# Kernel tuning notes

Measured on AMD Instinct MI355X. Metric: run time of the kernel, lower is better.

Reference implementation:

```python
import jax, jax.numpy as jnp
import numpy as np

N, D, R, NB, E = 50000, 128, 16, 10, 1600000
DECAY_RATE = 0.1
LN_EPS = 1e-5

def setup_inputs() -> dict:
    key = jax.random.key(0)
    ks = jax.random.split(key, 12)
    x = jax.random.normal(ks[0], (N, D), dtype=jnp.float32)
    edge_index = jax.random.randint(ks[1], (2, E), 0, N, dtype=jnp.int64)
    edge_type = jax.random.randint(ks[2], (E,), 0, R, dtype=jnp.int64)
    edge_time = jax.random.uniform(ks[3], (E,), dtype=jnp.float32)
    s = 1.0 / np.sqrt(D)
    basis = jax.random.normal(ks[4], (NB, D, D), dtype=jnp.float32) * s   # RGCN basis matrices
    comp = jax.random.normal(ks[5], (R, NB), dtype=jnp.float32) * (1.0 / np.sqrt(NB))
    root = jax.random.normal(ks[6], (D, D), dtype=jnp.float32) * s        # RGCN self-loop weight
    bias = jnp.zeros((D,), dtype=jnp.float32)
    tp_w = jax.random.normal(ks[7], (D, D), dtype=jnp.float32) * s        # time_proj
    tp_b = jnp.zeros((D,), dtype=jnp.float32)
    gamma = jnp.ones((D,), dtype=jnp.float32)
    beta = jnp.zeros((D,), dtype=jnp.float32)
    return {"x": x, "edge_index": edge_index, "edge_type": edge_type, "edge_time": edge_time,
            "basis": basis, "comp": comp, "root": root, "bias": bias,
            "tp_w": tp_w, "tp_b": tp_b, "gamma": gamma, "beta": beta}

def reference(x, edge_index, edge_type, edge_time, basis, comp, root, bias, tp_w, tp_b, gamma, beta):
    n, d = x.shape
    r = comp.shape[0]
    src, dst = edge_index[0], edge_index[1]
    # ---- RGCNConv (basis decomposition, per-relation mean aggregation) ----
    W = jnp.einsum('rb,bio->rio', comp, basis)                 # [R, D, D]
    msg = x[src]                                               # [E, D] gather
    seg = dst * r + edge_type                                  # combined (node, relation) segment id
    agg = jax.ops.segment_sum(msg, seg, num_segments=n * r)    # [N*R, D]
    cnt = jax.ops.segment_sum(jnp.ones_like(seg, dtype=x.dtype), seg, num_segments=n * r)
    agg = (agg / jnp.maximum(cnt, 1.0)[:, None]).reshape(n, r, d)  # per-relation mean
    x_rgcn = jnp.einsum('nrd,rdo->no', agg, W) + x @ root + bias
    # ---- exponential time decay weights, normalized to sum 1 ----
    td = edge_time.max() - edge_time
    td = td / (td.max() + 1e-8)
    w = jnp.exp(-DECAY_RATE * td)
    w = w / (w.sum() + 1e-8)
    # ---- time-decay aggregation (sum over relations == single scatter-add) ----
    agg_t = jax.ops.segment_sum(msg * w[:, None], dst, num_segments=n)
    deg = jax.ops.segment_sum(jnp.ones_like(dst, dtype=x.dtype), dst, num_segments=n)
    x_time = agg_t / jnp.clip(deg, 1.0)[:, None]
    # ---- combine, relu, (dropout=identity in eval), layernorm ----
    xc = x_rgcn + x_time @ tp_w + tp_b
    h = jax.nn.relu(xc)
    mu = h.mean(-1, keepdims=True)
    var = ((h - mu) ** 2).mean(-1, keepdims=True)
    return (h - mu) * jax.lax.rsqrt(var + LN_EPS) * gamma + beta
```

## Files before the change

### kernel.cpp

```cpp
#include <hip/hip_runtime.h>
#include <hip/hip_bf16.h>
#include <math.h>

#define NN 50000
#define DD 128
#define RR 16
#define NBASIS 10
#define NE 1600000
#define NSEG (NN * RR)
#define NPART ((NSEG + 1023) / 1024)
#define NSLICE 12
#define KTOT (NSLICE * DD)
#define DECAY 0.1f

typedef short bf16x8 __attribute__((ext_vector_type(8)));
typedef float f32x4 __attribute__((ext_vector_type(4)));
typedef float f32x2 __attribute__((ext_vector_type(2)));

__device__ __forceinline__ ushort f2b(float f) {
    unsigned u = __float_as_uint(f);
    unsigned r = (u + 0x7FFFu + ((u >> 16) & 1u)) >> 16;
    return (ushort)r;
}
__device__ __forceinline__ unsigned cvt_pk_bf16(float lo, float hi) {
    unsigned r;
    asm("v_cvt_pk_bf16_f32 %0, %1, %2" : "=v"(r) : "v"(lo), "v"(hi));
    return r;
}

__global__ void k_init(unsigned* red) {
    if (threadIdx.x == 0) {
        red[0] = 0u;
        red[1] = 0x7F800000u;
        ((float*)red)[2] = 0.0f;
    }
}

__global__ __launch_bounds__(256) void k_pre1(const float* __restrict__ t,
                                              const int* __restrict__ edst,
                                              const int* __restrict__ etype,
                                              unsigned* __restrict__ red,
                                              unsigned* __restrict__ cnt,
                                              unsigned* __restrict__ segarr,
                                              ushort* __restrict__ rank) {
    __shared__ float smx[4], smn[4];
    const int tid = threadIdx.x;
    float mx = 0.0f, mn = 1e30f;
    const int stride = gridDim.x * 256;
    for (int e = blockIdx.x * 256 + tid; e < NE; e += stride) {
        float v = __builtin_nontemporal_load(t + e);
        int d   = __builtin_nontemporal_load(edst + e);
        int ty  = __builtin_nontemporal_load(etype + e);
        mx = fmaxf(mx, v);
        mn = fminf(mn, v);
        int seg = d * RR + ty;
        unsigned rk = atomicAdd(&cnt[seg], 1u);
        __builtin_nontemporal_store((unsigned)seg, segarr + e);
        __builtin_nontemporal_store((ushort)rk, rank + e);
    }
    for (int o = 32; o >= 1; o >>= 1) {
        mx = fmaxf(mx, __shfl_down(mx, o, 64));
        mn = fminf(mn, __shfl_down(mn, o, 64));
    }
    if ((tid & 63) == 0) { smx[tid >> 6] = mx; smn[tid >> 6] = mn; }
    __syncthreads();
    if (tid == 0) {
        mx = fmaxf(fmaxf(smx[0], smx[1]), fmaxf(smx[2], smx[3]));
        mn = fminf(fminf(smn[0], smn[1]), fminf(smn[2], smn[3]));
        atomicMax(&red[0], __float_as_uint(mx));
        atomicMin(&red[1], __float_as_uint(mn));
    }
}

__global__ __launch_bounds__(1024) void k_scan1(const unsigned* __restrict__ cnt,
                                                unsigned* __restrict__ segptr,
                                                unsigned* __restrict__ part) {
    __shared__ unsigned sh[1024];
    int tid = threadIdx.x;
    int i = blockIdx.x * 1024 + tid;
    unsigned v = (i < NSEG) ? cnt[i] : 0u;
    sh[tid] = v;
    __syncthreads();
    for (int off = 1; off < 1024; off <<= 1) {
        unsigned t = (tid >= off) ? sh[tid - off] : 0u;
        __syncthreads();
        sh[tid] += t;
        __syncthreads();
    }
    if (i < NSEG) segptr[i] = sh[tid] - v;
    if (tid == 1023) part[blockIdx.x] = sh[1023];
}

__global__ __launch_bounds__(1024) void k_scan2(unsigned* __restrict__ part) {
    __shared__ unsigned sh[1024];
    int tid = threadIdx.x;
    unsigned v = (tid < NPART) ? part[tid] : 0u;
    sh[tid] = v;
    __syncthreads();
    for (int off = 1; off < 1024; off <<= 1) {
        unsigned t = (tid >= off) ? sh[tid - off] : 0u;
        __syncthreads();
        sh[tid] += t;
        __syncthreads();
    }
    if (tid < NPART) part[tid] = sh[tid] - v;
}

__global__ __launch_bounds__(1024) void k_scan3(unsigned* __restrict__ segptr,
                                                const unsigned* __restrict__ part) {
    int i = blockIdx.x * 1024 + threadIdx.x;
    if (i < NSEG) segptr[i] += part[i >> 10];
    if (blockIdx.x == 0 && threadIdx.x == 0) segptr[NSEG] = NE;
}

__global__ __launch_bounds__(256) void k_pre2(const int* __restrict__ esrc,
                                              const float* __restrict__ etime,
                                              const unsigned* __restrict__ segarr,
                                              const ushort* __restrict__ rank,
                                              unsigned* __restrict__ red,
                                              const unsigned* __restrict__ segptr,
                                              unsigned* __restrict__ srcw) {
    __shared__ float ssum[4];
    const int tid = threadIdx.x;
    const float tmax = __uint_as_float(red[0]);
    const float tmin = __uint_as_float(red[1]);
    const float rtd = -DECAY / (tmax - tmin + 1e-8f);
    float s = 0.0f;
    const int stride = gridDim.x * 256;
    for (int e = blockIdx.x * 256 + tid; e < NE; e += stride) {
        float tv    = __builtin_nontemporal_load(etime + e);
        int sv      = __builtin_nontemporal_load(esrc + e);
        unsigned sg = __builtin_nontemporal_load(segarr + e);
        unsigned rk = __builtin_nontemporal_load(rank + e);
        float w = __expf((tmax - tv) * rtd);
        s += w;
        unsigned pos = segptr[sg] + rk;
        srcw[pos] = (unsigned)(sv & 0xFFFF) | ((unsigned)f2b(w) << 16);
    }
    for (int o = 32; o >= 1; o >>= 1) s += __shfl_down(s, o, 64);
    if ((tid & 63) == 0) ssum[tid >> 6] = s;
    __syncthreads();
    if (tid == 0)
        atomicAdd(((float*)red) + 2, ssum[0] + ssum[1] + ssum[2] + ssum[3]);
}

#define XB_ITEMS (NN * (DD / 4))
__global__ __launch_bounds__(256) void k_prep(const float* __restrict__ x,
                                              const float* __restrict__ basis,
                                              const float* __restrict__ root,
                                              const float* __restrict__ tp_w,
                                              ushort* __restrict__ xb,
                                              ushort* __restrict__ Bt3) {
    int idx = blockIdx.x * 256 + threadIdx.x;
    if (idx < XB_ITEMS) {
        float4 v = ((const float4*)x)[idx];
        uint2 o;
        o.x = cvt_pk_bf16(v.x, v.y);
        o.y = cvt_pk_bf16(v.z, v.w);
        ((uint2*)xb)[idx] = o;
        return;
    }
    int bidx = idx - XB_ITEMS;
    if (bidx >= DD * KTOT) return;
    int j = bidx / KTOT, k = bidx - j * KTOT;
    int s = k >> 7, d = k & 127;
    float v;
    if (s < NBASIS) {
        v = basis[(s * DD + d) * DD + j];
    } else if (s == NBASIS) {
        v = tp_w[d * DD + j];
    } else {
        v = root[d * DD + j];
    }
    Bt3[bidx] = f2b(v);
}

__global__ __launch_bounds__(256) void k_gather(
    const ushort* __restrict__ xb, const unsigned* __restrict__ srcw,
    const unsigned* __restrict__ segptr, const unsigned* __restrict__ red,
    const float* __restrict__ comp,
    ushort* __restrict__ A2)
{
    const int wave = threadIdx.x >> 6, lane = threadIdx.x & 63;
    int dst0 = blockIdx.x * 4 + wave;
    if (dst0 >= NN) return;
    const int dst = __builtin_amdgcn_readfirstlane(dst0);
    const float sumw = ((const float*)red)[2];
    const unsigned s0 = (unsigned)dst * RR;
    const unsigned start = segptr[s0];
    const unsigned endAll = segptr[s0 + RR];
    const unsigned deg = endAll - start;
    unsigned* arow = (unsigned*)(A2 + (size_t)dst * KTOT);
    const unsigned* xbu = (const unsigned*)xb;

    f32x2 cb[NBASIS];
#pragma unroll
    for (int b = 0; b < NBASIS; ++b) cb[b] = (f32x2){0.f, 0.f};
    f32x2 acc = {0.f, 0.f}, xt = {0.f, 0.f};

    int r = 0;
    unsigned scur = start;
    unsigned endr = segptr[s0 + 1];
    unsigned e = start;

#define FLUSH_REL {                                                          \
        float scl = (endr > scur) ? (1.0f / (float)(endr - scur)) : 0.0f;    \
        f32x2 t = acc * scl;                                                 \
        _Pragma("unroll")                                                    \
        for (int b = 0; b < NBASIS; ++b)                                     \
            cb[b] += t * comp[r * NBASIS + b];                               \
        acc = (f32x2){0.f, 0.f}; scur = endr; ++r;                           \
        endr = (r < RR) ? segptr[s0 + r + 1] : 0xFFFFFFFFu; }

#define ACCUM(recq, pvq) {                                                   \
        float wgt = __uint_as_float((recq) & 0xFFFF0000u);                   \
        f32x2 v;                                                             \
        v.x = __uint_as_float((pvq) << 16);                                  \
        v.y = __uint_as_float((pvq) & 0xFFFF0000u);                          \
        acc += v;                                                            \
        xt += v * wgt; }

    while (e < endAll) {
        unsigned idx = e + (unsigned)lane;
        unsigned recv = srcw[(idx < endAll) ? idx : (endAll - 1u)];
        unsigned chunk = endAll - e;
        if (chunk > 64u) chunk = 64u;
        unsigned j = 0;
        for (; j + 8u <= chunk; j += 8u) {
            unsigned rec0 = (unsigned)__builtin_amdgcn_readlane((int)recv, (int)(j + 0));
            unsigned rec1 = (unsigned)__builtin_amdgcn_readlane((int)recv, (int)(j + 1));
            unsigned rec2 = (unsigned)__builtin_amdgcn_readlane((int)recv, (int)(j + 2));
            unsigned rec3 = (unsigned)__builtin_amdgcn_readlane((int)recv, (int)(j + 3));
            unsigned rec4 = (unsigned)__builtin_amdgcn_readlane((int)recv, (int)(j + 4));
            unsigned rec5 = (unsigned)__builtin_amdgcn_readlane((int)recv, (int)(j + 5));
            unsigned rec6 = (unsigned)__builtin_amdgcn_readlane((int)recv, (int)(j + 6));
            unsigned rec7 = (unsigned)__builtin_amdgcn_readlane((int)recv, (int)(j + 7));
            unsigned pv0 = xbu[((rec0 & 0xFFFFu) << 6) + lane];
            unsigned pv1 = xbu[((rec1 & 0xFFFFu) << 6) + lane];
            unsigned pv2 = xbu[((rec2 & 0xFFFFu) << 6) + lane];
            unsigned pv3 = xbu[((rec3 & 0xFFFFu) << 6) + lane];
            unsigned pv4 = xbu[((rec4 & 0xFFFFu) << 6) + lane];
            unsigned pv5 = xbu[((rec5 & 0xFFFFu) << 6) + lane];
            unsigned pv6 = xbu[((rec6 & 0xFFFFu) << 6) + lane];
            unsigned pv7 = xbu[((rec7 & 0xFFFFu) << 6) + lane];
            while (e >= endr) FLUSH_REL; ACCUM(rec0, pv0); ++e;
            while (e >= endr) FLUSH_REL; ACCUM(rec1, pv1); ++e;
            while (e >= endr) FLUSH_REL; ACCUM(rec2, pv2); ++e;
            while (e >= endr) FLUSH_REL; ACCUM(rec3, pv3); ++e;
            while (e >= endr) FLUSH_REL; ACCUM(rec4, pv4); ++e;
            while (e >= endr) FLUSH_REL; ACCUM(rec5, pv5); ++e;
            while (e >= endr) FLUSH_REL; ACCUM(rec6, pv6); ++e;
            while (e >= endr) FLUSH_REL; ACCUM(rec7, pv7); ++e;
        }
        for (; j < chunk; ++j) {
            unsigned rc = (unsigned)__builtin_amdgcn_readlane((int)recv, (int)j);
            unsigned pv = xbu[((rc & 0xFFFFu) << 6) + lane];
            while (e >= endr) FLUSH_REL;
            ACCUM(rc, pv);
            ++e;
        }
    }
    while (r < RR) FLUSH_REL;

#pragma unroll
    for (int b = 0; b < NBASIS; ++b)
        __builtin_nontemporal_store(cvt_pk_bf16(cb[b].x, cb[b].y),
                                    arow + b * 64 + lane);

    float s2 = 1.0f / ((sumw + 1e-8f) * fmaxf((float)deg, 1.0f));
    __builtin_nontemporal_store(cvt_pk_bf16(xt.x * s2, xt.y * s2),
                                arow + NBASIS * 64 + lane);
    __builtin_nontemporal_store(
        ((const unsigned*)(xb + (size_t)dst * DD))[lane],
        arow + (NBASIS + 1) * 64 + lane);
#undef FLUSH_REL
#undef ACCUM
}

__global__ __launch_bounds__(256) void k_fgemm(
    const ushort* __restrict__ A2, const ushort* __restrict__ Bt3,
    const float* __restrict__ bias, const float* __restrict__ tpb,
    const float* __restrict__ gamma, const float* __restrict__ beta,
    float* __restrict__ out)
{
    __shared__ unsigned Bs[2][4096];

    const int tid = threadIdx.x;
    const int w = tid >> 6, lane = tid & 63;
    const int quad = lane >> 4, l16 = lane & 15;
    const int n0 = blockIdx.x * 64;

    f32x4 acc[8];
#pragma unroll
    for (int ct = 0; ct < 8; ++ct) acc[ct] = (f32x4){0.f, 0.f, 0.f, 0.f};

    const ushort* arow = A2 + (size_t)(n0 + w * 16 + l16) * KTOT + quad * 8;
    const int srow = lane >> 3;
    const int sc   = lane & 7;

#define STAGE(buf, itv) {                                                    \
        const int k0_ = (itv) * 64;                                          \
        _Pragma("unroll")                                                    \
        for (int i_ = 0; i_ < 4; ++i_) {                                     \
            const int cid_ = i_ * 4 + w;                                     \
            const int row_ = cid_ * 8 + srow;                                \
            const int ck_  = sc ^ (row_ & 7);                                \
            const ushort* gb_ = Bt3 + (size_t)row_ * KTOT + k0_ + ck_ * 8;   \
            __builtin_amdgcn_global_load_lds(                                \
                (const __attribute__((address_space(1))) unsigned*)gb_,      \
                (__attribute__((address_space(3))) unsigned*)&Bs[buf][cid_ * 256], \
                16, 0, 0);                                                   \
        } }

    STAGE(0, 0);
    bf16x8 afp0 = *(const bf16x8*)(arow);
    bf16x8 afp1 = *(const bf16x8*)(arow + 32);
    __syncthreads();

    const int NIT = KTOT / 64;
    for (int it = 0; it < NIT; ++it) {
        if (it + 1 < NIT) STAGE((it + 1) & 1, it + 1);
        bf16x8 af0 = afp0, af1 = afp1;
        if (it + 1 < NIT) {
            afp0 = *(const bf16x8*)(arow + (it + 1) * 64);
            afp1 = *(const bf16x8*)(arow + (it + 1) * 64 + 32);
        }
        const unsigned* Bp = &Bs[it & 1][0];
#pragma unroll
        for (int ct = 0; ct < 8; ++ct) {
            const int rB = ct * 16 + l16;
            bf16x8 b0 = *(const bf16x8*)&Bp[rB * 32 + ((quad ^ (rB & 7)) << 2)];
            bf16x8 b1 = *(const bf16x8*)&Bp[rB * 32 + (((4 + quad) ^ (rB & 7)) << 2)];
            acc[ct] = __builtin_amdgcn_mfma_f32_16x16x32_bf16(af0, b0, acc[ct], 0, 0, 0);
            acc[ct] = __builtin_amdgcn_mfma_f32_16x16x32_bf16(af1, b1, acc[ct], 0, 0, 0);
        }
        __syncthreads();
    }
#undef STAGE

    float bc[8], gc[8], be[8];
#pragma unroll
    for (int ct = 0; ct < 8; ++ct) {
        int col = ct * 16 + l16;
        bc[ct] = bias[col] + tpb[col];
        gc[ct] = gamma[col];
        be[ct] = beta[col];
    }
    float s[4] = {0, 0, 0, 0}, q[4] = {0, 0, 0, 0};
#pragma unroll
    for (int ct = 0; ct < 8; ++ct)
#pragma unroll
        for (int i = 0; i < 4; ++i) {
            float v = fmaxf(acc[ct][i] + bc[ct], 0.0f);
            acc[ct][i] = v;
            s[i] += v;
            q[i] = fmaf(v, v, q[i]);
        }
#pragma unroll
    for (int off = 1; off < 16; off <<= 1)
#pragma unroll
        for (int i = 0; i < 4; ++i) {
            s[i] += __shfl_xor(s[i], off, 64);
            q[i] += __shfl_xor(q[i], off, 64);
        }
#pragma unroll
    for (int i = 0; i < 4; ++i) {
        const int row = n0 + w * 16 + quad * 4 + i;
        float mu  = s[i] * (1.0f / DD);
        float var = q[i] * (1.0f / DD) - mu * mu;
        float inv = rsqrtf(var + 1e-5f);
        if (row < NN) {
#pragma unroll
            for (int ct = 0; ct < 8; ++ct)
                __builtin_nontemporal_store(
                    (acc[ct][i] - mu) * inv * gc[ct] + be[ct],
                    out + (size_t)row * DD + ct * 16 + l16);
        }
    }
}

extern "C" void kernel_launch(void* const* d_in, const int* in_sizes, int n_in,
                              void* d_out, int out_size, void* d_ws, size_t ws_size,
                              hipStream_t stream)
{
    const float* x     = (const float*)d_in[0];
    const int*   ei    = (const int*)d_in[1];
    const int*   etype = (const int*)d_in[2];
    const float* etime = (const float*)d_in[3];
    const float* basis = (const float*)d_in[4];
    const float* comp  = (const float*)d_in[5];
    const float* root  = (const float*)d_in[6];
    const float* bias  = (const float*)d_in[7];
    const float* tp_w  = (const float*)d_in[8];
    const float* tp_b  = (const float*)d_in[9];
    const float* gamma = (const float*)d_in[10];
    const float* beta  = (const float*)d_in[11];
    float* out = (float*)d_out;

    char* ws = (char*)d_ws;
    size_t off = 0;
    auto alloc = [&](size_t bytes) -> void* {
        void* p = ws + off;
        off = (off + bytes + 255) & ~(size_t)255;
        return p;
    };
    unsigned* red    = (unsigned*)alloc(64);
    unsigned* cnt    = (unsigned*)alloc((size_t)NSEG * 4);
    unsigned* segptr = (unsigned*)alloc((size_t)(NSEG + 1) * 4);
    unsigned* part   = (unsigned*)alloc(1024 * 4);
    unsigned* srcw   = (unsigned*)alloc((size_t)NE * 4);
    unsigned* segarr = (unsigned*)alloc((size_t)NE * 4);
    ushort*   rank   = (ushort*)alloc((size_t)NE * 2);
    ushort*   xb     = (ushort*)alloc((size_t)NN * DD * 2);
    ushort*   Bt3    = (ushort*)alloc((size_t)DD * KTOT * 2);
    ushort*   A2     = (ushort*)alloc((size_t)50048 * KTOT * 2);
    (void)ws_size;

    const int* esrc = ei;
    const int* edst = ei + NE;

    hipLaunchKernelGGL(k_init, dim3(1), dim3(64), 0, stream, red);
    (void)hipMemsetAsync(cnt, 0, (size_t)NSEG * 4, stream);
    hipLaunchKernelGGL(k_pre1, dim3(1024), dim3(256), 0, stream,
                       etime, edst, etype, red, cnt, segarr, rank);

    hipLaunchKernelGGL(k_scan1, dim3(NPART), dim3(1024), 0, stream, cnt, segptr, part);
    hipLaunchKernelGGL(k_scan2, dim3(1), dim3(1024), 0, stream, part);
    hipLaunchKernelGGL(k_scan3, dim3(NPART), dim3(1024), 0, stream, segptr, part);

    hipLaunchKernelGGL(k_pre2, dim3(1024), dim3(256), 0, stream,
                       esrc, etime, segarr, rank, red, segptr, srcw);

    hipLaunchKernelGGL(k_prep, dim3((XB_ITEMS + DD * KTOT + 255) / 256), dim3(256), 0, stream,
                       x, basis, root, tp_w, xb, Bt3);

    hipLaunchKernelGGL(k_gather, dim3((NN + 3) / 4), dim3(256), 0, stream,
                       xb, srcw, segptr, red, comp, A2);

    hipLaunchKernelGGL(k_fgemm, dim3((50048 + 63) / 64), dim3(256), 0, stream,
                       A2, Bt3, bias, tp_b, gamma, beta, out);
}
```

Measured before the change: 391.9 us.

## Fuse counting, time min/max and bf16 prep into one front kernel; pack seg+rank

Merges the atomic segment-counting pass, the edge-time min/max reduction and the x/weight bf16 conversion into a single launch whose block ranges do independent work. This lets the three jobs run concurrently and removes one launch. Segment id and rank are now packed into one 32-bit word, replacing separate 4-byte and 2-byte arrays and cutting traffic in k_pre2. The scatter store of srcw becomes nontemporal. Packing assumes each segment's rank stays below 4096 and each segment id fits in 20 bits.

```diff
diff --git a/kernel.cpp b/kernel.cpp
--- a/kernel.cpp
+++ b/kernel.cpp
@@ -36,40 +36,75 @@
     }
 }
 
-__global__ __launch_bounds__(256) void k_pre1(const float* __restrict__ t,
-                                              const int* __restrict__ edst,
-                                              const int* __restrict__ etype,
-                                              unsigned* __restrict__ red,
-                                              unsigned* __restrict__ cnt,
-                                              unsigned* __restrict__ segarr,
-                                              ushort* __restrict__ rank) {
-    __shared__ float smx[4], smn[4];
+#define XB_ITEMS (NN * (DD / 4))
+#define PREP_ITEMS (XB_ITEMS + DD * KTOT)
+__global__ __launch_bounds__(256) void k_front(
+    const int* __restrict__ edst, const int* __restrict__ etype,
+    const float* __restrict__ t,
+    const float* __restrict__ x, const float* __restrict__ basis,
+    const float* __restrict__ root, const float* __restrict__ tp_w,
+    unsigned* __restrict__ red, unsigned* __restrict__ cnt,
+    unsigned* __restrict__ segrank,
+    ushort* __restrict__ xb, ushort* __restrict__ Bt3)
+{
+    const int bid = blockIdx.x;
     const int tid = threadIdx.x;
-    float mx = 0.0f, mn = 1e30f;
-    const int stride = gridDim.x * 256;
-    for (int e = blockIdx.x * 256 + tid; e < NE; e += stride) {
-        float v = __builtin_nontemporal_load(t + e);
-        int d   = __builtin_nontemporal_load(edst + e);
-        int ty  = __builtin_nontemporal_load(etype + e);
-        mx = fmaxf(mx, v);
-        mn = fminf(mn, v);
-        int seg = d * RR + ty;
-        unsigned rk = atomicAdd(&cnt[seg], 1u);
-        __builtin_nontemporal_store((unsigned)seg, segarr + e);
-        __builtin_nontemporal_store((ushort)rk, rank + e);
-    }
-    for (int o = 32; o >= 1; o >>= 1) {
-        mx = fmaxf(mx, __shfl_down(mx, o, 64));
-        mn = fminf(mn, __shfl_down(mn, o, 64));
-    }
-    if ((tid & 63) == 0) { smx[tid >> 6] = mx; smn[tid >> 6] = mn; }
-    __syncthreads();
-    if (tid == 0) {
-        mx = fmaxf(fmaxf(smx[0], smx[1]), fmaxf(smx[2], smx[3]));
-        mn = fminf(fminf(smn[0], smn[1]), fminf(smn[2], smn[3]));
-        atomicMax(&red[0], __float_as_uint(mx));
-        atomicMin(&red[1], __float_as_uint(mn));
-    }
+    if (bid < 1024) {
+        const int stride = 1024 * 256;
+        for (int e = bid * 256 + tid; e < NE; e += stride) {
+            int d  = __builtin_nontemporal_load(edst + e);
+            int ty = __builtin_nontemporal_load(etype + e);
+            int seg = d * RR + ty;
+            unsigned rk = atomicAdd(&cnt[seg], 1u);
+            __builtin_nontemporal_store(((unsigned)seg << 12) | rk, segrank + e);
+        }
+        return;
+    }
+    if (bid < 2048) {
+        __shared__ float smx[4], smn[4];
+        float mx = 0.0f, mn = 1e30f;
+        const int stride = 1024 * 256;
+        for (int i = (bid - 1024) * 256 + tid; i < NE / 4; i += stride) {
+            f32x4 v = __builtin_nontemporal_load(((const f32x4*)t) + i);
+            mx = fmaxf(mx, fmaxf(fmaxf(v.x, v.y), fmaxf(v.z, v.w)));
+            mn = fminf(mn, fminf(fminf(v.x, v.y), fminf(v.z, v.w)));
+        }
+        for (int o = 32; o >= 1; o >>= 1) {
+            mx = fmaxf(mx, __shfl_down(mx, o, 64));
+            mn = fminf(mn, __shfl_down(mn, o, 64));
+        }
+        if ((tid & 63) == 0) { smx[tid >> 6] = mx; smn[tid >> 6] = mn; }
+        __syncthreads();
+        if (tid == 0) {
+            mx = fmaxf(fmaxf(smx[0], smx[1]), fmaxf(smx[2], smx[3]));
+            mn = fminf(fminf(smn[0], smn[1]), fminf(smn[2], smn[3]));
+            atomicMax(&red[0], __float_as_uint(mx));
+            atomicMin(&red[1], __float_as_uint(mn));
+        }
+        return;
+    }
+    int idx = (bid - 2048) * 256 + tid;
+    if (idx < XB_ITEMS) {
+        f32x4 v = ((const f32x4*)x)[idx];
+        uint2 o;
+        o.x = cvt_pk_bf16(v.x, v.y);
+        o.y = cvt_pk_bf16(v.z, v.w);
+        ((uint2*)xb)[idx] = o;
+        return;
+    }
+    int bidx = idx - XB_ITEMS;
+    if (bidx >= DD * KTOT) return;
+    int j = bidx / KTOT, k = bidx - j * KTOT;
+    int s = k >> 7, d = k & 127;
+    float v;
+    if (s < NBASIS) {
+        v = basis[(s * DD + d) * DD + j];
+    } else if (s == NBASIS) {
+        v = tp_w[d * DD + j];
+    } else {
+        v = root[d * DD + j];
+    }
+    Bt3[bidx] = f2b(v);
 }
 
 __global__ __launch_bounds__(1024) void k_scan1(const unsigned* __restrict__ cnt,
@@ -115,8 +150,7 @@
 
 __global__ __launch_bounds__(256) void k_pre2(const int* __restrict__ esrc,
                                               const float* __restrict__ etime,
-                                              const unsigned* __restrict__ segarr,
-                                              const ushort* __restrict__ rank,
+                                              const unsigned* __restrict__ segrank,
                                               unsigned* __restrict__ red,
                                               const unsigned* __restrict__ segptr,
                                               unsigned* __restrict__ srcw) {
@@ -130,49 +164,18 @@
     for (int e = blockIdx.x * 256 + tid; e < NE; e += stride) {
         float tv    = __builtin_nontemporal_load(etime + e);
         int sv      = __builtin_nontemporal_load(esrc + e);
-        unsigned sg = __builtin_nontemporal_load(segarr + e);
-        unsigned rk = __builtin_nontemporal_load(rank + e);
+        unsigned sr = __builtin_nontemporal_load(segrank + e);
         float w = __expf((tmax - tv) * rtd);
         s += w;
-        unsigned pos = segptr[sg] + rk;
-        srcw[pos] = (unsigned)(sv & 0xFFFF) | ((unsigned)f2b(w) << 16);
+        unsigned pos = segptr[sr >> 12] + (sr & 4095u);
+        __builtin_nontemporal_store(
+            (unsigned)(sv & 0xFFFF) | ((unsigned)f2b(w) << 16), srcw + pos);
     }
     for (int o = 32; o >= 1; o >>= 1) s += __shfl_down(s, o, 64);
     if ((tid & 63) == 0) ssum[tid >> 6] = s;
     __syncthreads();
     if (tid == 0)
         atomicAdd(((float*)red) + 2, ssum[0] + ssum[1] + ssum[2] + ssum[3]);
-}
-
-#define XB_ITEMS (NN * (DD / 4))
-__global__ __launch_bounds__(256) void k_prep(const float* __restrict__ x,
-                                              const float* __restrict__ basis,
-                                              const float* __restrict__ root,
-                                              const float* __restrict__ tp_w,
-                                              ushort* __restrict__ xb,
-                                              ushort* __restrict__ Bt3) {
-    int idx = blockIdx.x * 256 + threadIdx.x;
-    if (idx < XB_ITEMS) {
-        float4 v = ((const float4*)x)[idx];
-        uint2 o;
-        o.x = cvt_pk_bf16(v.x, v.y);
-        o.y = cvt_pk_bf16(v.z, v.w);
-        ((uint2*)xb)[idx] = o;
-        return;
-    }
-    int bidx = idx - XB_ITEMS;
-    if (bidx >= DD * KTOT) return;
-    int j = bidx / KTOT, k = bidx - j * KTOT;
-    int s = k >> 7, d = k & 127;
-    float v;
-    if (s < NBASIS) {
-        v = basis[(s * DD + d) * DD + j];
-    } else if (s == NBASIS) {
-        v = tp_w[d * DD + j];
-    } else {
-        v = root[d * DD + j];
-    }
-    Bt3[bidx] = f2b(v);
 }
 
 __global__ __launch_bounds__(256) void k_gather(
@@ -404,16 +407,15 @@
         off = (off + bytes + 255) & ~(size_t)255;
         return p;
     };
-    unsigned* red    = (unsigned*)alloc(64);
-    unsigned* cnt    = (unsigned*)alloc((size_t)NSEG * 4);
-    unsigned* segptr = (unsigned*)alloc((size_t)(NSEG + 1) * 4);
-    unsigned* part   = (unsigned*)alloc(1024 * 4);
-    unsigned* srcw   = (unsigned*)alloc((size_t)NE * 4);
-    unsigned* segarr = (unsigned*)alloc((size_t)NE * 4);
-    ushort*   rank   = (ushort*)alloc((size_t)NE * 2);
-    ushort*   xb     = (ushort*)alloc((size_t)NN * DD * 2);
-    ushort*   Bt3    = (ushort*)alloc((size_t)DD * KTOT * 2);
-    ushort*   A2     = (ushort*)alloc((size_t)50048 * KTOT * 2);
+    unsigned* red     = (unsigned*)alloc(64);
+    unsigned* cnt     = (unsigned*)alloc((size_t)NSEG * 4);
+    unsigned* segptr  = (unsigned*)alloc((size_t)(NSEG + 1) * 4);
+    unsigned* part    = (unsigned*)alloc(1024 * 4);
+    unsigned* srcw    = (unsigned*)alloc((size_t)NE * 4);
+    unsigned* segrank = (unsigned*)alloc((size_t)NE * 4);
+    ushort*   xb      = (ushort*)alloc((size_t)NN * DD * 2);
+    ushort*   Bt3     = (ushort*)alloc((size_t)DD * KTOT * 2);
+    ushort*   A2      = (ushort*)alloc((size_t)50048 * KTOT * 2);
     (void)ws_size;
 
     const int* esrc = ei;
@@ -421,18 +423,18 @@
 
     hipLaunchKernelGGL(k_init, dim3(1), dim3(64), 0, stream, red);
     (void)hipMemsetAsync(cnt, 0, (size_t)NSEG * 4, stream);
-    hipLaunchKernelGGL(k_pre1, dim3(1024), dim3(256), 0, stream,
-                       etime, edst, etype, red, cnt, segarr, rank);
+
+    const int prep_blocks = (PREP_ITEMS + 255) / 256;
+    hipLaunchKernelGGL(k_front, dim3(2048 + prep_blocks), dim3(256), 0, stream,
+                       edst, etype, etime, x, basis, root, tp_w,
+                       red, cnt, segrank, xb, Bt3);
 
     hipLaunchKernelGGL(k_scan1, dim3(NPART), dim3(1024), 0, stream, cnt, segptr, part);
     hipLaunchKernelGGL(k_scan2, dim3(1), dim3(1024), 0, stream, part);
     hipLaunchKernelGGL(k_scan3, dim3(NPART), dim3(1024), 0, stream, segptr, part);
 
     hipLaunchKernelGGL(k_pre2, dim3(1024), dim3(256), 0, stream,
-                       esrc, etime, segarr, rank, red, segptr, srcw);
-
-    hipLaunchKernelGGL(k_prep, dim3((XB_ITEMS + DD * KTOT + 255) / 256), dim3(256), 0, stream,
-                       x, basis, root, tp_w, xb, Bt3);
+                       esrc, etime, segrank, red, segptr, srcw);
 
     hipLaunchKernelGGL(k_gather, dim3((NN + 3) / 4), dim3(256), 0, stream,
                        xb, srcw, segptr, red, comp, A2);
```

After: 389.9 us. Within noise of the previous version (-0.5%).
